# Performance work log

Hardware: AMD Instinct MI355X
Metric: run time of the kernel (lower is better)

## Reference

```python
import jax, jax.numpy as jnp
import numpy as np

NUM_SEQS = 32
KV_LEN = 2048          # cached context length per sequence
NUM_HEADS = 16
HEAD_SIZE = 128
SCALE = 0.08838834764831845  # 1/sqrt(HEAD_SIZE)
TOTAL_SLOTS = NUM_SEQS * KV_LEN


def setup_inputs() -> dict:
    key = jax.random.key(0)
    kq, kk, kv, kc = jax.random.split(key, 4)
    q = jax.random.normal(kq, (NUM_SEQS, NUM_HEADS, HEAD_SIZE), dtype=jnp.float32)
    k = jax.random.normal(kk, (NUM_SEQS, NUM_HEADS, HEAD_SIZE), dtype=jnp.float32)
    v = jax.random.normal(kv, (NUM_SEQS, NUM_HEADS, HEAD_SIZE), dtype=jnp.float32)
    kv_cache = jax.random.normal(kc, (2, TOTAL_SLOTS, NUM_HEADS, HEAD_SIZE), dtype=jnp.float32)
    # each sequence owns slots [i*KV_LEN, (i+1)*KV_LEN); new token written at the last slot
    slot_mapping = jnp.arange(NUM_SEQS, dtype=jnp.int64) * KV_LEN + (KV_LEN - 1)
    return {"q": q, "k": k, "v": v, "kv_cache": kv_cache, "slot_mapping": slot_mapping}


def reference(q, k, v, kv_cache, slot_mapping):
    # 1) reshape_and_cache: scatter new k/v into the paged cache at slot_mapping
    kv_cache = kv_cache.at[0, slot_mapping].set(k)
    kv_cache = kv_cache.at[1, slot_mapping].set(v)
    # 2) paged attention decode: each query attends over its own contiguous slot range
    keys = kv_cache[0].reshape(NUM_SEQS, KV_LEN, NUM_HEADS, HEAD_SIZE)
    vals = kv_cache[1].reshape(NUM_SEQS, KV_LEN, NUM_HEADS, HEAD_SIZE)
    scores = jnp.einsum("shd,sthd->sht", q, keys) * SCALE  # [seqs, heads, kv_len]
    probs = jax.nn.softmax(scores, axis=-1)
    out = jnp.einsum("sht,sthd->shd", probs, vals)         # [seqs, heads, head_size]
    return out
```

## Files before the change

### kernel.cpp

```cpp
#include <hip/hip_runtime.h>

constexpr int NUM_SEQS  = 32;
constexpr int KV_LEN    = 2048;
constexpr int NUM_HEADS = 16;
constexpr int HEAD_SIZE = 128;
constexpr float SCALE   = 0.08838834764831845f;

constexpr int HSTRIDE = NUM_HEADS * HEAD_SIZE;
constexpr size_t KV_PLANE = (size_t)NUM_SEQS * KV_LEN * HSTRIDE;

__global__ __launch_bounds__(256, 4)
void paged_decode_kernel(const float* __restrict__ q,
                         const float* __restrict__ knew,
                         const float* __restrict__ vnew,
                         const float* __restrict__ kv,
                         const int*  __restrict__ slot_map,
                         float* __restrict__ out)
{
    const int bid  = blockIdx.x;
    const int s    = bid >> 4;
    const int h    = bid & (NUM_HEADS - 1);
    const int tid  = threadIdx.x;
    const int half = tid >> 5;
    const int lane = tid & 31;

    __shared__ float sc[KV_LEN];
    __shared__ float red[4];
    __shared__ float s_inv;
    __shared__ float part[8][HEAD_SIZE];

    const int qoff = (s * NUM_HEADS + h) * HEAD_SIZE;
    const float* kbase = kv + (size_t)s * KV_LEN * HSTRIDE + (size_t)h * HEAD_SIZE;
    const float* vbase = kbase + KV_PLANE;
    const int t_new = slot_map[s] - s * KV_LEN;

    const float4 qv = *reinterpret_cast<const float4*>(q + qoff + lane * 4);

    for (int base = 0; base < KV_LEN; base += 32) {
        const int t0 = base + half * 4;

        const float* p0 = (t0 + 0 == t_new) ? (knew + qoff) : (kbase + (size_t)(t0 + 0) * HSTRIDE);
        const float* p1 = (t0 + 1 == t_new) ? (knew + qoff) : (kbase + (size_t)(t0 + 1) * HSTRIDE);
        const float* p2 = (t0 + 2 == t_new) ? (knew + qoff) : (kbase + (size_t)(t0 + 2) * HSTRIDE);
        const float* p3 = (t0 + 3 == t_new) ? (knew + qoff) : (kbase + (size_t)(t0 + 3) * HSTRIDE);

        const float4 k0 = *reinterpret_cast<const float4*>(p0 + lane * 4);
        const float4 k1 = *reinterpret_cast<const float4*>(p1 + lane * 4);
        const float4 k2 = *reinterpret_cast<const float4*>(p2 + lane * 4);
        const float4 k3 = *reinterpret_cast<const float4*>(p3 + lane * 4);

        float d0 = fmaf(k0.x, qv.x, fmaf(k0.y, qv.y, fmaf(k0.z, qv.z, k0.w * qv.w)));
        float d1 = fmaf(k1.x, qv.x, fmaf(k1.y, qv.y, fmaf(k1.z, qv.z, k1.w * qv.w)));
        float d2 = fmaf(k2.x, qv.x, fmaf(k2.y, qv.y, fmaf(k2.z, qv.z, k2.w * qv.w)));
        float d3 = fmaf(k3.x, qv.x, fmaf(k3.y, qv.y, fmaf(k3.z, qv.z, k3.w * qv.w)));

        #pragma unroll
        for (int off = 16; off > 0; off >>= 1) {
            d0 += __shfl_xor(d0, off);
            d1 += __shfl_xor(d1, off);
            d2 += __shfl_xor(d2, off);
            d3 += __shfl_xor(d3, off);
        }
        if (lane == 0) {
            sc[t0 + 0] = d0 * SCALE;
            sc[t0 + 1] = d1 * SCALE;
            sc[t0 + 2] = d2 * SCALE;
            sc[t0 + 3] = d3 * SCALE;
        }
    }
    __syncthreads();

    float m = -1e30f;
    #pragma unroll
    for (int t = tid; t < KV_LEN; t += 256) m = fmaxf(m, sc[t]);
    #pragma unroll
    for (int off = 32; off > 0; off >>= 1) m = fmaxf(m, __shfl_xor(m, off));
    if ((tid & 63) == 0) red[tid >> 6] = m;
    __syncthreads();
    const float mblk = fmaxf(fmaxf(red[0], red[1]), fmaxf(red[2], red[3]));

    float lsum = 0.f;
    #pragma unroll
    for (int t = tid; t < KV_LEN; t += 256) {
        const float e = __expf(sc[t] - mblk);
        sc[t] = e;
        lsum += e;
    }
    #pragma unroll
    for (int off = 32; off > 0; off >>= 1) lsum += __shfl_xor(lsum, off);
    __syncthreads();
    if ((tid & 63) == 0) red[tid >> 6] = lsum;
    __syncthreads();
    if (tid == 0) s_inv = 1.0f / (red[0] + red[1] + red[2] + red[3]);
    __syncthreads();
    const float inv = s_inv;

    float4 acc = make_float4(0.f, 0.f, 0.f, 0.f);
    for (int base = 0; base < KV_LEN; base += 32) {
        const int t0 = base + half * 4;

        const float* p0 = (t0 + 0 == t_new) ? (vnew + qoff) : (vbase + (size_t)(t0 + 0) * HSTRIDE);
        const float* p1 = (t0 + 1 == t_new) ? (vnew + qoff) : (vbase + (size_t)(t0 + 1) * HSTRIDE);
        const float* p2 = (t0 + 2 == t_new) ? (vnew + qoff) : (vbase + (size_t)(t0 + 2) * HSTRIDE);
        const float* p3 = (t0 + 3 == t_new) ? (vnew + qoff) : (vbase + (size_t)(t0 + 3) * HSTRIDE);

        const float4 v0 = *reinterpret_cast<const float4*>(p0 + lane * 4);
        const float4 v1 = *reinterpret_cast<const float4*>(p1 + lane * 4);
        const float4 v2 = *reinterpret_cast<const float4*>(p2 + lane * 4);
        const float4 v3 = *reinterpret_cast<const float4*>(p3 + lane * 4);

        const float w0 = sc[t0 + 0];
        const float w1 = sc[t0 + 1];
        const float w2 = sc[t0 + 2];
        const float w3 = sc[t0 + 3];

        acc.x = fmaf(w0, v0.x, acc.x); acc.y = fmaf(w0, v0.y, acc.y);
        acc.z = fmaf(w0, v0.z, acc.z); acc.w = fmaf(w0, v0.w, acc.w);
        acc.x = fmaf(w1, v1.x, acc.x); acc.y = fmaf(w1, v1.y, acc.y);
        acc.z = fmaf(w1, v1.z, acc.z); acc.w = fmaf(w1, v1.w, acc.w);
        acc.x = fmaf(w2, v2.x, acc.x); acc.y = fmaf(w2, v2.y, acc.y);
        acc.z = fmaf(w2, v2.z, acc.z); acc.w = fmaf(w2, v2.w, acc.w);
        acc.x = fmaf(w3, v3.x, acc.x); acc.y = fmaf(w3, v3.y, acc.y);
        acc.z = fmaf(w3, v3.z, acc.z); acc.w = fmaf(w3, v3.w, acc.w);
    }

    *reinterpret_cast<float4*>(&part[half][lane * 4]) = acc;
    __syncthreads();

    if (tid < HEAD_SIZE) {
        float o = 0.f;
        #pragma unroll
        for (int i = 0; i < 8; ++i) o += part[i][tid];
        out[qoff + tid] = o * inv;
    }
}

extern "C" void kernel_launch(void* const* d_in, const int* in_sizes, int n_in,
                              void* d_out, int out_size, void* d_ws, size_t ws_size,
                              hipStream_t stream) {
    const float* q    = (const float*)d_in[0];
    const float* k    = (const float*)d_in[1];
    const float* v    = (const float*)d_in[2];
    const float* kv   = (const float*)d_in[3];
    const int*   slot = (const int*)d_in[4];
    float* out = (float*)d_out;

    dim3 grid(NUM_SEQS * NUM_HEADS);
    dim3 block(256);
    hipLaunchKernelGGL(paged_decode_kernel, grid, block, 0, stream,
                       q, k, v, kv, slot, out);
}
```

Before: 1.280 ms.

## Split KV length across blocks with flash-decoding partial softmax and reduce kernel

Each sequence-head's KV range is split into four chunks, each processed by its own block that writes a local max, sum and unnormalized output to workspace. A second small kernel merges the partials with log-sum-exp rescaling. This raises the grid from 512 to 2048 blocks so more CUs stream the cache concurrently, at the cost of an extra launch and workspace traffic. If no workspace is provided, it falls back to the single-pass kernel.

After: 1.299 ms. About the same (+1.5%).

```diff
diff --git a/kernel.cpp b/kernel.cpp
--- a/kernel.cpp
+++ b/kernel.cpp
@@ -9,35 +9,46 @@
 constexpr int HSTRIDE = NUM_HEADS * HEAD_SIZE;
 constexpr size_t KV_PLANE = (size_t)NUM_SEQS * KV_LEN * HSTRIDE;
 
-__global__ __launch_bounds__(256, 4)
-void paged_decode_kernel(const float* __restrict__ q,
-                         const float* __restrict__ knew,
-                         const float* __restrict__ vnew,
-                         const float* __restrict__ kv,
-                         const int*  __restrict__ slot_map,
-                         float* __restrict__ out)
+constexpr int NPART   = 4;
+constexpr int PSTRIDE = HEAD_SIZE + 2;
+
+template <int NP>
+__global__ __launch_bounds__(256, 8)
+void paged_decode_partial(const float* __restrict__ q,
+                          const float* __restrict__ knew,
+                          const float* __restrict__ vnew,
+                          const float* __restrict__ kv,
+                          const int*  __restrict__ slot_map,
+                          float* __restrict__ ws,
+                          float* __restrict__ out)
 {
-    const int bid  = blockIdx.x;
-    const int s    = bid >> 4;
-    const int h    = bid & (NUM_HEADS - 1);
+    constexpr int CH = KV_LEN / NP;
+
+    const int bid = blockIdx.x;
+    const int c   = bid & (NP - 1);
+    const int sh  = bid / NP;
+    const int s   = sh >> 4;
+    const int h   = sh & (NUM_HEADS - 1);
+
     const int tid  = threadIdx.x;
     const int half = tid >> 5;
     const int lane = tid & 31;
 
-    __shared__ float sc[KV_LEN];
+    __shared__ float sc[CH];
     __shared__ float red[4];
-    __shared__ float s_inv;
     __shared__ float part[8][HEAD_SIZE];
 
-    const int qoff = (s * NUM_HEADS + h) * HEAD_SIZE;
+    const int qoff = sh * HEAD_SIZE;
     const float* kbase = kv + (size_t)s * KV_LEN * HSTRIDE + (size_t)h * HEAD_SIZE;
     const float* vbase = kbase + KV_PLANE;
     const int t_new = slot_map[s] - s * KV_LEN;
+    const int tbeg  = c * CH;
 
     const float4 qv = *reinterpret_cast<const float4*>(q + qoff + lane * 4);
 
-    for (int base = 0; base < KV_LEN; base += 32) {
-        const int t0 = base + half * 4;
+    for (int base = 0; base < CH; base += 32) {
+        const int l0 = base + half * 4;
+        const int t0 = tbeg + l0;
 
         const float* p0 = (t0 + 0 == t_new) ? (knew + qoff) : (kbase + (size_t)(t0 + 0) * HSTRIDE);
         const float* p1 = (t0 + 1 == t_new) ? (knew + qoff) : (kbase + (size_t)(t0 + 1) * HSTRIDE);
@@ -62,17 +73,17 @@
             d3 += __shfl_xor(d3, off);
         }
         if (lane == 0) {
-            sc[t0 + 0] = d0 * SCALE;
-            sc[t0 + 1] = d1 * SCALE;
-            sc[t0 + 2] = d2 * SCALE;
-            sc[t0 + 3] = d3 * SCALE;
+            sc[l0 + 0] = d0 * SCALE;
+            sc[l0 + 1] = d1 * SCALE;
+            sc[l0 + 2] = d2 * SCALE;
+            sc[l0 + 3] = d3 * SCALE;
         }
     }
     __syncthreads();
 
     float m = -1e30f;
     #pragma unroll
-    for (int t = tid; t < KV_LEN; t += 256) m = fmaxf(m, sc[t]);
+    for (int t = tid; t < CH; t += 256) m = fmaxf(m, sc[t]);
     #pragma unroll
     for (int off = 32; off > 0; off >>= 1) m = fmaxf(m, __shfl_xor(m, off));
     if ((tid & 63) == 0) red[tid >> 6] = m;
@@ -81,7 +92,7 @@
 
     float lsum = 0.f;
     #pragma unroll
-    for (int t = tid; t < KV_LEN; t += 256) {
+    for (int t = tid; t < CH; t += 256) {
         const float e = __expf(sc[t] - mblk);
         sc[t] = e;
         lsum += e;
@@ -91,13 +102,12 @@
     __syncthreads();
     if ((tid & 63) == 0) red[tid >> 6] = lsum;
     __syncthreads();
-    if (tid == 0) s_inv = 1.0f / (red[0] + red[1] + red[2] + red[3]);
-    __syncthreads();
-    const float inv = s_inv;
+    const float lloc = red[0] + red[1] + red[2] + red[3];
 
     float4 acc = make_float4(0.f, 0.f, 0.f, 0.f);
-    for (int base = 0; base < KV_LEN; base += 32) {
-        const int t0 = base + half * 4;
+    for (int base = 0; base < CH; base += 32) {
+        const int l0 = base + half * 4;
+        const int t0 = tbeg + l0;
 
         const float* p0 = (t0 + 0 == t_new) ? (vnew + qoff) : (vbase + (size_t)(t0 + 0) * HSTRIDE);
         const float* p1 = (t0 + 1 == t_new) ? (vnew + qoff) : (vbase + (size_t)(t0 + 1) * HSTRIDE);
@@ -109,10 +119,10 @@
         const float4 v2 = *reinterpret_cast<const float4*>(p2 + lane * 4);
         const float4 v3 = *reinterpret_cast<const float4*>(p3 + lane * 4);
 
-        const float w0 = sc[t0 + 0];
-        const float w1 = sc[t0 + 1];
-        const float w2 = sc[t0 + 2];
-        const float w3 = sc[t0 + 3];
+        const float w0 = sc[l0 + 0];
+        const float w1 = sc[l0 + 1];
+        const float w2 = sc[l0 + 2];
+        const float w3 = sc[l0 + 3];
 
         acc.x = fmaf(w0, v0.x, acc.x); acc.y = fmaf(w0, v0.y, acc.y);
         acc.z = fmaf(w0, v0.z, acc.z); acc.w = fmaf(w0, v0.w, acc.w);
@@ -127,12 +137,47 @@
     *reinterpret_cast<float4*>(&part[half][lane * 4]) = acc;
     __syncthreads();
 
-    if (tid < HEAD_SIZE) {
-        float o = 0.f;
-        #pragma unroll
-        for (int i = 0; i < 8; ++i) o += part[i][tid];
-        out[qoff + tid] = o * inv;
-    }
+    if constexpr (NP == 1) {
+        if (tid < HEAD_SIZE) {
+            float o = 0.f;
+            #pragma unroll
+            for (int i = 0; i < 8; ++i) o += part[i][tid];
+            out[qoff + tid] = o / lloc;
+        }
+    } else {
+        float* rec = ws + (size_t)bid * PSTRIDE;
+        if (tid < HEAD_SIZE) {
+            float o = 0.f;
+            #pragma unroll
+            for (int i = 0; i < 8; ++i) o += part[i][tid];
+            rec[2 + tid] = o;
+        }
+        if (tid == 0) {
+            rec[0] = mblk;
+            rec[1] = lloc;
+        }
+    }
+}
+
+__global__ __launch_bounds__(128)
+void paged_decode_reduce(const float* __restrict__ ws, float* __restrict__ out)
+{
+    const int sh = blockIdx.x;
+    const int i  = threadIdx.x;
+    const float* rec0 = ws + (size_t)sh * NPART * PSTRIDE;
+
+    float M = -1e30f;
+    #pragma unroll
+    for (int c = 0; c < NPART; ++c) M = fmaxf(M, rec0[c * PSTRIDE]);
+
+    float L = 0.f, o = 0.f;
+    #pragma unroll
+    for (int c = 0; c < NPART; ++c) {
+        const float w = __expf(rec0[c * PSTRIDE] - M);
+        L = fmaf(rec0[c * PSTRIDE + 1], w, L);
+        o = fmaf(rec0[c * PSTRIDE + 2 + i], w, o);
+    }
+    out[sh * HEAD_SIZE + i] = o / L;
 }
 
 extern "C" void kernel_launch(void* const* d_in, const int* in_sizes, int n_in,
@@ -145,8 +190,17 @@
     const int*   slot = (const int*)d_in[4];
     float* out = (float*)d_out;
 
-    dim3 grid(NUM_SEQS * NUM_HEADS);
-    dim3 block(256);
-    hipLaunchKernelGGL(paged_decode_kernel, grid, block, 0, stream,
-                       q, k, v, kv, slot, out);
+    const size_t need = (size_t)NUM_SEQS * NUM_HEADS * NPART * PSTRIDE * sizeof(float);
+    if (d_ws != nullptr && ws_size >= need) {
+        dim3 grid1(NUM_SEQS * NUM_HEADS * NPART);
+        hipLaunchKernelGGL(paged_decode_partial<NPART>, grid1, dim3(256), 0, stream,
+                           q, k, v, kv, slot, (float*)d_ws, out);
+        dim3 grid2(NUM_SEQS * NUM_HEADS);
+        hipLaunchKernelGGL(paged_decode_reduce, grid2, dim3(128), 0, stream,
+                           (float*)d_ws, out);
+    } else {
+        dim3 grid(NUM_SEQS * NUM_HEADS);
+        hipLaunchKernelGGL(paged_decode_partial<1>, grid, dim3(256), 0, stream,
+                           q, k, v, kv, slot, nullptr, out);
+    }
 }
```
